# Kernel optimization log

Hardware: AMD Instinct MI355X
Metric: run time of the kernel (lower is better)

## Reference

```python
import jax, jax.numpy as jnp
import numpy as np

B, N = 1, 6            # batch, cameras -> BN = 6
FC, FH, FW = 256, 32, 88
D_ST, D_END, D_STEP = 1.0, 60.0, 1.0
C_OUT = 128
X, Y = 128, 128        # BEV grid
BN_EPS = 1e-3


def setup_inputs() -> dict:
    key = jax.random.key(0)
    ks = jax.random.split(key, 12)
    BNc = B * N
    inp = {
        'relative_depth': jax.random.uniform(ks[0], (BNc, 1, FH, FW), jnp.float32),
        'img_feats': jax.random.normal(ks[1], (BNc, FC, FH, FW), jnp.float32),
        'voxel_ids': jax.random.randint(ks[2], (BNc, 59, FH, FW), 0, X * Y, jnp.int32),
        # aligner + bin converter params (scalars)
        'log_scale': jnp.log(jnp.float32(50.0)),
        'shift': jnp.float32(5.0),
        'log_sigma': jnp.log(jnp.float32(2.0)),
        # feature_net params
        'conv1_w': jax.random.normal(ks[3], (FC, FC, 3, 3), jnp.float32) * 0.02,
        'conv1_b': jnp.zeros((FC,), jnp.float32),
        'bn1_g': jnp.ones((FC,), jnp.float32),
        'bn1_b': jnp.zeros((FC,), jnp.float32),
        'bn1_m': jnp.zeros((FC,), jnp.float32),
        'bn1_v': jnp.ones((FC,), jnp.float32),
        'conv2_w': jax.random.normal(ks[4], (FC, FC, 3, 3), jnp.float32) * 0.02,
        'conv2_b': jnp.zeros((FC,), jnp.float32),
        'bn2_g': jnp.ones((FC,), jnp.float32),
        'bn2_b': jnp.zeros((FC,), jnp.float32),
        'bn2_m': jnp.zeros((FC,), jnp.float32),
        'bn2_v': jnp.ones((FC,), jnp.float32),
        'conv3_w': jax.random.normal(ks[5], (C_OUT, FC, 1, 1), jnp.float32) * 0.02,
        'conv3_b': jnp.zeros((C_OUT,), jnp.float32),
    }
    return inp


def _conv2d(x, w, b, pad):
    y = jax.lax.conv_general_dilated(x, w, (1, 1), [(pad, pad), (pad, pad)],
                                     dimension_numbers=('NCHW', 'OIHW', 'NCHW'))
    return y + b[None, :, None, None]


def _bn_eval(x, g, b, m, v):
    inv = g / jnp.sqrt(v + BN_EPS)
    return (x - m[None, :, None, None]) * inv[None, :, None, None] + b[None, :, None, None]


def reference(relative_depth, img_feats, voxel_ids, log_scale, shift, log_sigma,
              conv1_w, conv1_b, bn1_g, bn1_b, bn1_m, bn1_v,
              conv2_w, conv2_b, bn2_g, bn2_b, bn2_m, bn2_v,
              conv3_w, conv3_b):
    bins = jnp.arange(D_ST, D_END, D_STEP, dtype=jnp.float32)  # (D,) = 59
    D = bins.shape[0]

    # 1) aligner: relative -> metric depth
    metric = jnp.clip(jnp.exp(log_scale) * relative_depth + shift, 0.5, 150.0)  # (BN,1,H,W)

    # 2) Laplace-kernel depth-bin distribution
    sigma = jnp.clip(jnp.exp(log_sigma), 0.1, 20.0)
    logits = -jnp.abs(metric - bins[None, :, None, None]) / sigma  # (BN,D,H,W)
    depth_dist = jax.nn.softmax(logits, axis=1)

    # 3) feature head (convs in eval-mode BN)
    h = jax.nn.relu(_bn_eval(_conv2d(img_feats, conv1_w, conv1_b, 1), bn1_g, bn1_b, bn1_m, bn1_v))
    h = jax.nn.relu(_bn_eval(_conv2d(h, conv2_w, conv2_b, 1), bn2_g, bn2_b, bn2_m, bn2_v))
    feat = _conv2d(h, conv3_w, conv3_b, 0)  # (BN,C,H,W)

    # 4) lift: outer product depth_dist x features -> (BN,C,D,H,W)
    volume = depth_dist[:, None] * feat[:, :, None]

    # 5) splat: scatter-sum frustum points into BEV voxel grid (B,C,X,Y)
    BNc = volume.shape[0]
    pts = jnp.transpose(volume, (0, 2, 3, 4, 1)).reshape(-1, C_OUT)  # (BN*D*H*W, C)
    b_idx = (jnp.arange(BNc, dtype=jnp.int32) // N)[:, None, None, None]
    seg = (b_idx * (X * Y) + voxel_ids).reshape(-1)
    bev = jax.ops.segment_sum(pts, seg, num_segments=B * X * Y)  # (B*X*Y, C)
    bev = jnp.transpose(bev.reshape(B, X, Y, C_OUT), (0, 3, 1, 2))  # (B,C,X,Y)
    return bev
```

## Files before the change

### kernel.cpp

```cpp
#include <hip/hip_runtime.h>
#include <math.h>

#define HW   2816
#define IMGS 6
#define DD   59
#define NV   16384
#define COUT 128
#define NPIX (IMGS*HW)
#define WCUT 1e-5f
#define CAP  128

typedef _Float16 half8  __attribute__((ext_vector_type(8)));
typedef _Float16 half2v __attribute__((ext_vector_type(2)));
typedef float f32x4 __attribute__((ext_vector_type(4)));

__device__ __forceinline__ void glds16(const _Float16* g, const _Float16* l){
    __builtin_amdgcn_global_load_lds(
        (const __attribute__((address_space(1))) void*)g,
        (__attribute__((address_space(3))) void*)l, 16, 0, 0);
}


struct DepthCtx { float metric, inv, mx, rs; };

__device__ __forceinline__ DepthCtx depth_ctx(float relv, float lsc, float shf, float lsg){
    DepthCtx c;
    float scale = expf(lsc);
    float sig   = fminf(fmaxf(expf(lsg), 0.1f), 20.f);
    c.inv = 1.f/sig;
    c.metric = fminf(fmaxf(scale*relv + shf, 0.5f), 150.f);
    float nb = fminf(fmaxf(rintf(c.metric), 1.f), 59.f);
    c.mx = -fabsf(c.metric - nb)*c.inv;
    float sum = 0.f;
    for (int d = 0; d < DD; ++d)
        sum += expf(-fabsf(c.metric - (float)(d+1))*c.inv - c.mx);
    c.rs = 1.f/sum;
    return c;
}


__device__ __forceinline__ void wsplit_body(const float* __restrict__ w,
                                            _Float16* __restrict__ wh,
                                            int idx, int CO, int CI, int KK){
    if (idx >= CO*CI*KK) return;
    int co  = idx/(CI*KK);
    int r   = idx - co*CI*KK;
    int ci  = r/KK;
    int tap = r - ci*KK;
    wh[((size_t)tap*CO + co)*CI + ci] = (_Float16)w[idx];
}

__global__ void prep_kernel(int* __restrict__ cursor,
                            const float* __restrict__ w1, _Float16* __restrict__ wh1,
                            const float* __restrict__ w2, _Float16* __restrict__ wh2,
                            const float* __restrict__ w3, _Float16* __restrict__ wh3,
                            const float* __restrict__ c1b, const float* __restrict__ g1,
                            const float* __restrict__ bb1, const float* __restrict__ m1,
                            const float* __restrict__ v1,
                            const float* __restrict__ c2b, const float* __restrict__ g2,
                            const float* __restrict__ bb2, const float* __restrict__ m2,
                            const float* __restrict__ v2,
                            float* __restrict__ s1, float* __restrict__ t1,
                            float* __restrict__ s2, float* __restrict__ t2,
                            const float* __restrict__ rel, const float* __restrict__ lsc,
                            const float* __restrict__ shf, const float* __restrict__ lsg,
                            float4* __restrict__ dparams,
                            const float* __restrict__ imgf, _Float16* __restrict__ inH){
    __shared__ float tile[32][33];
    int b = blockIdx.x, t = threadIdx.x;
    if (b < 65){
        int i = b*256 + t;
        if (i < NV + 64) cursor[i] = 0;
    } else if (b < 2369){
        wsplit_body(w1, wh1, (b-65)*256 + t, 256, 256, 9);
    } else if (b < 4673){
        wsplit_body(w2, wh2, (b-2369)*256 + t, 256, 256, 9);
    } else if (b < 4801){
        wsplit_body(w3, wh3, (b-4673)*256 + t, 128, 256, 1);
    } else if (b == 4801){
        int c = t;
        float i1 = g1[c]/sqrtf(v1[c]+1e-3f);
        s1[c] = i1; t1[c] = (c1b[c]-m1[c])*i1 + bb1[c];
        float i2 = g2[c]/sqrtf(v2[c]+1e-3f);
        s2[c] = i2; t2[c] = (c2b[c]-m2[c])*i2 + bb2[c];
    } else if (b < 4868){
        int g = (b-4802)*256 + t;
        if (g < NPIX){
            DepthCtx c = depth_ctx(rel[g], lsc[0], shf[0], lsg[0]);
            dparams[g] = make_float4(c.metric, c.inv, c.mx, c.rs);
        }
    } else {
        int bb = b - 4868;
        int img = bb/704, rem = bb - img*704;
        int p0 = (rem % 88)*32, c0 = (rem/88)*32;
        int tx = t & 31, ty = t >> 5;
#pragma unroll
        for (int k = 0; k < 4; ++k)
            tile[ty + 8*k][tx] = imgf[((size_t)(img*256 + c0 + ty + 8*k))*HW + p0 + tx];
        __syncthreads();
#pragma unroll
        for (int k = 0; k < 4; ++k)
            inH[((size_t)(img*HW + p0 + ty + 8*k))*256 + c0 + tx] = (_Float16)tile[tx][ty + 8*k];
    }
}

template<int TAPS, bool BN_RELU, int COT>
__global__ __launch_bounds__(256,4) void conv_mfma(
    const _Float16* __restrict__ in,
    const _Float16* __restrict__ wT,
    const float* __restrict__ scale, const float* __restrict__ bias,
    _Float16* __restrict__ out,
    const _Float16* __restrict__ zp)
{
    __shared__ __align__(16) _Float16 As[4096];
    __shared__ __align__(16) _Float16 Bs[8192];

    const int t    = threadIdx.x;
    const int wave = t >> 6;
    const int lane = t & 63;
    const int g    = lane >> 4;
    const int l15  = lane & 15;
    const int wr   = wave >> 1, wc = wave & 1;
    const int g0   = blockIdx.x*64;
    const int img  = g0/HW;
    const int pbase= g0 - img*HW;
    const int n0   = blockIdx.y*128;
    const int imgbase = img*HW;
    const int NK   = TAPS*4;

    int aPy[2], aPx[2], aOct[2], aLo[2];
#pragma unroll
    for (int i = 0; i < 2; ++i){
        int s = i*256 + t;
        int row = s >> 3;
        aOct[i] = ((s & 7) ^ (row & 7))*8;
        int p = pbase + row;
        aPy[i] = p/88; aPx[i] = p - aPy[i]*88;
        aLo[i] = (i*256 + wave*64)*8;
    }
    int bOff[4], bLo[4];
#pragma unroll
    for (int i = 0; i < 4; ++i){
        int s = i*256 + t;
        int row = s >> 3;
        bOff[i] = (n0 + row)*256 + ((s & 7) ^ (row & 7))*8;
        bLo[i]  = (i*256 + wave*64)*8;
    }
    int arow[2], brow[4];
#pragma unroll
    for (int f = 0; f < 2; ++f) arow[f] = wr*32 + f*16 + l15;
#pragma unroll
    for (int f = 0; f < 4; ++f) brow[f] = wc*64 + f*16 + l15;

    f32x4 acc[2][4];
#pragma unroll
    for (int i = 0; i < 2; ++i)
#pragma unroll
        for (int j = 0; j < 4; ++j) acc[i][j] = (f32x4){0.f,0.f,0.f,0.f};

    for (int kk = 0; kk < NK; ++kk){
        const int tap = kk >> 2, ci0 = (kk & 3) << 6;
        const int dy = (TAPS == 9) ? tap/3 - 1 : 0;
        const int dx = (TAPS == 9) ? tap - (tap/3)*3 - 1 : 0;

        __syncthreads();
#pragma unroll
        for (int i = 0; i < 2; ++i){
            int yy = aPy[i] + dy, xx = aPx[i] + dx;
            bool valid = ((unsigned)yy < 32u) && ((unsigned)xx < 88u);
            const _Float16* src = valid
                ? in + (size_t)(imgbase + yy*88 + xx)*256 + ci0 + aOct[i] : zp;
            glds16(src, As + aLo[i]);
        }
        const _Float16* wb = wT + (size_t)tap*COT*256 + ci0;
#pragma unroll
        for (int i = 0; i < 4; ++i)
            glds16(wb + bOff[i], Bs + bLo[i]);
        __syncthreads();

#pragma unroll
        for (int ks = 0; ks < 2; ++ks){
            half8 a[2], bf[4];
#pragma unroll
            for (int f = 0; f < 2; ++f)
                a[f] = *(const half8*)(As + (arow[f]*8 + (((ks*4 + g) ^ (arow[f] & 7))))*8);
#pragma unroll
            for (int f = 0; f < 4; ++f)
                bf[f] = *(const half8*)(Bs + (brow[f]*8 + (((ks*4 + g) ^ (brow[f] & 7))))*8);
#pragma unroll
            for (int mi = 0; mi < 2; ++mi)
#pragma unroll
            for (int ni = 0; ni < 4; ++ni)
                acc[mi][ni] = __builtin_amdgcn_mfma_f32_16x16x32_f16(a[mi], bf[ni], acc[mi][ni], 0,0,0);
        }
    }

#pragma unroll
    for (int ni = 0; ni < 4; ++ni){
        int co = n0 + wc*64 + ni*16 + l15;
        float sc = BN_RELU ? scale[co] : 0.f;
        float bi = bias[co];
#pragma unroll
        for (int mi = 0; mi < 2; ++mi){
            f32x4 v = acc[mi][ni];
            int rb = g0 + wr*32 + mi*16 + g*4;
#pragma unroll
            for (int r = 0; r < 4; ++r){
                float y;
                if (BN_RELU) y = fmaxf(fmaf(v[r], sc, bi), 0.f);
                else         y = v[r] + bi;
                out[(size_t)(rb + r)*COT + co] = (_Float16)y;
            }
        }
    }
}

__global__ void fill_kernel(const float4* __restrict__ dparams,
                            const int* __restrict__ vids,
                            int* __restrict__ cursor, int2* __restrict__ records){
    int tid = blockIdx.x*256 + threadIdx.x;
    if (tid >= NPIX*DD) return;
    int d  = tid/NPIX;
    int pp = tid - d*NPIX;
    int bn = pp/HW;
    int p  = pp - bn*HW;
    float4 c = dparams[pp];
    float w = expf(-fabsf(c.x - (float)(d+1))*c.y - c.z)*c.w;
    if (w >= WCUT){
        int v = vids[(bn*DD + d)*HW + p];
        int pos = atomicAdd(&cursor[v], 1);
        if (pos < CAP) records[v*CAP + pos] = make_int2(pp, __float_as_int(w));
    }
}

__global__ __launch_bounds__(256,8) void gather_kernel(
    const int2* __restrict__ records, const int* __restrict__ cursor,
    const _Float16* __restrict__ feat16, float* __restrict__ bev_t){
    int v    = blockIdx.x*4 + (threadIdx.x >> 6);
    int lane = threadIdx.x & 63;
    int n = min(cursor[v], CAP);
    const int2* rec = records + v*CAP;
    float a0 = 0.f, a1 = 0.f;
    int i = 0;
    for (; i + 8 <= n; i += 8){
        int2 r[8];
#pragma unroll
        for (int j = 0; j < 8; ++j) r[j] = rec[i+j];
        half2v f[8];
#pragma unroll
        for (int j = 0; j < 8; ++j)
            f[j] = *(const half2v*)(feat16 + (size_t)r[j].x*COUT + lane*2);
#pragma unroll
        for (int j = 0; j < 8; ++j){
            float w = __int_as_float(r[j].y);
            a0 = fmaf(w, (float)f[j][0], a0);
            a1 = fmaf(w, (float)f[j][1], a1);
        }
    }
    for (; i < n; ++i){
        int2 r = rec[i];
        half2v f = *(const half2v*)(feat16 + (size_t)r.x*COUT + lane*2);
        float w = __int_as_float(r.y);
        a0 = fmaf(w, (float)f[0], a0); a1 = fmaf(w, (float)f[1], a1);
    }
    *(float2*)(bev_t + (size_t)v*COUT + lane*2) = make_float2(a0, a1);
}

__global__ void transpose_out(const float* __restrict__ bev_t, float* __restrict__ out){
    __shared__ float tile[32][33];
    int v0 = blockIdx.x*32, c0 = blockIdx.y*32;
    int tx = threadIdx.x & 31, ty = threadIdx.x >> 5;
#pragma unroll
    for (int k = 0; k < 4; ++k)
        tile[ty + 8*k][tx] = bev_t[(size_t)(v0 + ty + 8*k)*COUT + c0 + tx];
    __syncthreads();
#pragma unroll
    for (int k = 0; k < 4; ++k)
        out[(size_t)(c0 + ty + 8*k)*NV + v0 + tx] = tile[tx][ty + 8*k];
}


extern "C" void kernel_launch(void* const* d_in, const int* in_sizes, int n_in,
                              void* d_out, int out_size, void* d_ws, size_t ws_size,
                              hipStream_t stream){
    const float* rel  = (const float*)d_in[0];
    const float* imgf = (const float*)d_in[1];
    const int*   vids = (const int*)d_in[2];
    const float* lsc  = (const float*)d_in[3];
    const float* shf  = (const float*)d_in[4];
    const float* lsg  = (const float*)d_in[5];
    const float* w1   = (const float*)d_in[6];
    const float* b1   = (const float*)d_in[7];
    const float* g1   = (const float*)d_in[8];
    const float* bb1  = (const float*)d_in[9];
    const float* m1   = (const float*)d_in[10];
    const float* v1   = (const float*)d_in[11];
    const float* w2   = (const float*)d_in[12];
    const float* b2   = (const float*)d_in[13];
    const float* g2   = (const float*)d_in[14];
    const float* bb2  = (const float*)d_in[15];
    const float* m2   = (const float*)d_in[16];
    const float* v2   = (const float*)d_in[17];
    const float* w3   = (const float*)d_in[18];
    const float* b3   = (const float*)d_in[19];

    char* ws = (char*)d_ws;
    size_t o = 0;
    auto alloc = [&](size_t bytes)->char*{
        char* p = ws + o;
        o += (bytes + 255) & ~(size_t)255;
        return p;
    };
    int* cursor = (int*)alloc((size_t)(NV + 64)*4);
    const _Float16* zpad16 = (const _Float16*)(cursor + NV);
    float4* dparams = (float4*)alloc((size_t)NPIX*16);

    _Float16* wT1 = (_Float16*)alloc((size_t)9*256*256*2);
    _Float16* wT2 = (_Float16*)alloc((size_t)9*256*256*2);
    _Float16* wT3 = (_Float16*)alloc((size_t)128*256*2);
    float* s1 = (float*)alloc(256*4);
    float* t1 = (float*)alloc(256*4);
    float* s2 = (float*)alloc(256*4);
    float* t2 = (float*)alloc(256*4);

    _Float16* in0 = (_Float16*)alloc((size_t)NPIX*256*2);
    _Float16* h1  = (_Float16*)alloc((size_t)NPIX*256*2);
    _Float16* feat16 = (_Float16*)alloc((size_t)NPIX*COUT*2);
    float* bev_t  = (float*)alloc((size_t)NV*COUT*4);
    int2* records = (int2*)alloc((size_t)NV*CAP*8);
    _Float16* h2 = in0;

    prep_kernel<<<9092,256,0,stream>>>(cursor,
        w1, wT1, w2, wT2, w3, wT3,
        b1,g1,bb1,m1,v1, b2,g2,bb2,m2,v2, s1,t1,s2,t2,
        rel, lsc, shf, lsg, dparams, imgf, in0);

    conv_mfma<9,true ,256><<<dim3(264,2),256,0,stream>>>(in0, wT1, s1, t1, h1, zpad16);
    conv_mfma<9,true ,256><<<dim3(264,2),256,0,stream>>>(h1,  wT2, s2, t2, h2, zpad16);
    conv_mfma<1,false,128><<<dim3(264,1),256,0,stream>>>(h2,  wT3, s1, b3, feat16, zpad16);

    fill_kernel<<<3894,256,0,stream>>>(dparams, vids, cursor, records);
    gather_kernel<<<4096,256,0,stream>>>(records, cursor, feat16, bev_t);
    transpose_out<<<dim3(512,4),256,0,stream>>>(bev_t, (float*)d_out);
}
```

Before: 237.9 us.

## Fuse conv1 with depth-weight fill in one launch and raise conv occupancy

```diff
diff --git a/kernel.cpp b/kernel.cpp
--- a/kernel.cpp
+++ b/kernel.cpp
@@ -9,6 +9,8 @@
 #define NPIX (IMGS*HW)
 #define WCUT 1e-5f
 #define CAP  128
+#define NCONV1 528
+#define NFILL  3894
 
 typedef _Float16 half8  __attribute__((ext_vector_type(8)));
 typedef _Float16 half2v __attribute__((ext_vector_type(2)));
@@ -41,13 +43,13 @@
 
 __device__ __forceinline__ void wsplit_body(const float* __restrict__ w,
                                             _Float16* __restrict__ wh,
-                                            int idx, int CO, int CI, int KK){
-    if (idx >= CO*CI*KK) return;
-    int co  = idx/(CI*KK);
-    int r   = idx - co*CI*KK;
-    int ci  = r/KK;
-    int tap = r - ci*KK;
-    wh[((size_t)tap*CO + co)*CI + ci] = (_Float16)w[idx];
+                                            int o, int CO, int CI, int KK){
+    if (o >= CO*CI*KK) return;
+    int tap = o/(CO*CI);
+    int r   = o - tap*CO*CI;
+    int co  = r/CI;
+    int ci  = r - co*CI;
+    wh[o] = (_Float16)w[(co*CI + ci)*KK + tap];
 }
 
 __global__ void prep_kernel(int* __restrict__ cursor,
@@ -105,7 +107,7 @@
 }
 
 template<int TAPS, bool BN_RELU, int COT>
-__global__ __launch_bounds__(256,4) void conv_mfma(
+__device__ __forceinline__ void conv_body(int bx, int by,
     const _Float16* __restrict__ in,
     const _Float16* __restrict__ wT,
     const float* __restrict__ scale, const float* __restrict__ bias,
@@ -121,10 +123,10 @@
     const int g    = lane >> 4;
     const int l15  = lane & 15;
     const int wr   = wave >> 1, wc = wave & 1;
-    const int g0   = blockIdx.x*64;
+    const int g0   = bx*64;
     const int img  = g0/HW;
     const int pbase= g0 - img*HW;
-    const int n0   = blockIdx.y*128;
+    const int n0   = by*128;
     const int imgbase = img*HW;
     const int NK   = TAPS*4;
 
@@ -215,10 +217,10 @@
     }
 }
 
-__global__ void fill_kernel(const float4* __restrict__ dparams,
-                            const int* __restrict__ vids,
-                            int* __restrict__ cursor, int2* __restrict__ records){
-    int tid = blockIdx.x*256 + threadIdx.x;
+__device__ __forceinline__ void fill_body(int bb, int t,
+    const float4* __restrict__ dparams, const int* __restrict__ vids,
+    int* __restrict__ cursor, int2* __restrict__ records){
+    int tid = bb*256 + t;
     if (tid >= NPIX*DD) return;
     int d  = tid/NPIX;
     int pp = tid - d*NPIX;
@@ -230,6 +232,28 @@
         int v = vids[(bn*DD + d)*HW + p];
         int pos = atomicAdd(&cursor[v], 1);
         if (pos < CAP) records[v*CAP + pos] = make_int2(pp, __float_as_int(w));
+    }
+}
+
+template<int TAPS, bool BN_RELU, int COT>
+__global__ __launch_bounds__(256,6) void conv_mfma(
+    const _Float16* __restrict__ in, const _Float16* __restrict__ wT,
+    const float* __restrict__ scale, const float* __restrict__ bias,
+    _Float16* __restrict__ out, const _Float16* __restrict__ zp){
+    conv_body<TAPS,BN_RELU,COT>(blockIdx.x, blockIdx.y, in, wT, scale, bias, out, zp);
+}
+
+__global__ __launch_bounds__(256,6) void conv1_fill_kernel(
+    const _Float16* __restrict__ in, const _Float16* __restrict__ wT,
+    const float* __restrict__ scale, const float* __restrict__ bias,
+    _Float16* __restrict__ out, const _Float16* __restrict__ zp,
+    const float4* __restrict__ dparams, const int* __restrict__ vids,
+    int* __restrict__ cursor, int2* __restrict__ records){
+    int b = blockIdx.x;
+    if (b < NCONV1){
+        conv_body<9,true,256>(b % 264, b / 264, in, wT, scale, bias, out, zp);
+    } else {
+        fill_body(b - NCONV1, threadIdx.x, dparams, vids, cursor, records);
     }
 }
 
@@ -335,11 +359,11 @@
         b1,g1,bb1,m1,v1, b2,g2,bb2,m2,v2, s1,t1,s2,t2,
         rel, lsc, shf, lsg, dparams, imgf, in0);
 
-    conv_mfma<9,true ,256><<<dim3(264,2),256,0,stream>>>(in0, wT1, s1, t1, h1, zpad16);
+    conv1_fill_kernel<<<NCONV1 + NFILL,256,0,stream>>>(
+        in0, wT1, s1, t1, h1, zpad16, dparams, vids, cursor, records);
     conv_mfma<9,true ,256><<<dim3(264,2),256,0,stream>>>(h1,  wT2, s2, t2, h2, zpad16);
     conv_mfma<1,false,128><<<dim3(264,1),256,0,stream>>>(h2,  wT3, s1, b3, feat16, zpad16);
 
-    fill_kernel<<<3894,256,0,stream>>>(dparams, vids, cursor, records);
     gather_kernel<<<4096,256,0,stream>>>(records, cursor, feat16, bev_t);
     transpose_out<<<dim3(512,4),256,0,stream>>>(bev_t, (float*)d_out);
 }
```

Result: no change. 236.7 us (-0.5%).
